# Performance work log

Hardware: AMD Instinct MI355X
Metric: run time of the kernel (lower is better)

Reference implementation:

```python
import jax, jax.numpy as jnp
import numpy as np

D_CONV = 4
DT_RANK = 64
D_STATE = 16

def silu(v):
    return v * jax.nn.sigmoid(v)

def setup_inputs() -> dict:
    key = jax.random.key(0)
    ks = jax.random.split(key, 10)
    B, L, d_model, d_inner = 2, 2048, 1024, 2048
    def nrm(k, shape, scale):
        return jax.random.normal(k, shape, dtype=jnp.float32) * scale
    A = jnp.tile(jnp.arange(1, D_STATE + 1, dtype=jnp.float32), (d_inner, 1))
    return {
        'x': nrm(ks[0], (B, L, d_model), 1.0),
        'W_in': nrm(ks[1], (d_model, 2 * d_inner), d_model ** -0.5),
        'conv_w': nrm(ks[2], (d_inner, D_CONV), D_CONV ** -0.5),
        'conv_b': nrm(ks[3], (d_inner,), 0.02),
        'W_x': nrm(ks[4], (d_inner, DT_RANK + 2 * D_STATE), d_inner ** -0.5),
        'W_dt': nrm(ks[5], (DT_RANK, d_inner), DT_RANK ** -0.5),
        'b_dt': nrm(ks[6], (d_inner,), 0.02),
        'A_log': jnp.log(A),
        'D': jnp.ones((d_inner,), dtype=jnp.float32),
        'W_out': nrm(ks[7], (d_inner, d_model), d_inner ** -0.5),
    }

def reference(x, W_in, conv_w, conv_b, W_x, W_dt, b_dt, A_log, D, W_out):
    B, L, _ = x.shape
    d_inner = W_dt.shape[1]
    # input projection and gate split
    xz = x @ W_in                                   # [B, L, 2*d_inner]
    xb, z = jnp.split(xz, 2, axis=-1)
    # causal depthwise conv1d (pad left d_conv-1, then first L outputs)
    xp = jnp.pad(xb, ((0, 0), (D_CONV - 1, 0), (0, 0)))
    xc = sum(xp[:, k:k + L, :] * conv_w[:, k] for k in range(D_CONV)) + conv_b
    xb = silu(xc)                                   # [B, L, d_inner]
    # data-dependent SSM parameters
    x_dbl = xb @ W_x                                # [B, L, dt_rank + 2*d_state]
    dt_low, Bm, Cm = jnp.split(x_dbl, [DT_RANK, DT_RANK + D_STATE], axis=-1)
    dt = jax.nn.softplus(dt_low @ W_dt + b_dt)      # [B, L, d_inner]
    A = -jnp.exp(A_log)                             # [d_inner, d_state]

    def step(h, inp):
        dt_t, B_t, C_t, x_t = inp                   # [B,d_inner],[B,n],[B,n],[B,d_inner]
        dA = jnp.exp(A * dt_t[..., None])           # [B, d_inner, d_state]
        h = h * dA + (x_t * dt_t)[..., None] * B_t[:, None, :]
        y = jnp.einsum('bdn,bn->bd', h, C_t)
        return h, y

    xs = (dt.swapaxes(0, 1), Bm.swapaxes(0, 1), Cm.swapaxes(0, 1), xb.swapaxes(0, 1))
    h0 = jnp.zeros((B, d_inner, D_STATE), dtype=x.dtype)
    _, ys = jax.lax.scan(step, h0, xs)              # ys: [L, B, d_inner]
    y = ys.swapaxes(0, 1) + xb * D
    out = y * silu(z)
    return out @ W_out
```

## Files before the change

kernel.cpp:

```cpp
#include <hip/hip_runtime.h>
#include <hip/hip_bf16.h>


#define BATCH   2
#define SEQLEN  2048
#define DMODEL  1024
#define DINNER  2048
#define DCONV   4
#define DTRANK  64
#define DSTATE  16
#define BL      (BATCH * SEQLEN)
#define NXZ     (2 * DINNER)
#define XDBL_N  (DTRANK + 2 * DSTATE)
#define LCH     32
#define NCHUNK  (SEQLEN / LCH)
#define KSPLIT  8
#define KC      (DINNER / KSPLIT)
#define ALDS    264
#define KS_OUT  4
#define KCO     (DINNER / KS_OUT)

typedef __bf16 bf16x8 __attribute__((ext_vector_type(8)));
typedef __bf16 bf16x4 __attribute__((ext_vector_type(4)));
typedef float  floatx4 __attribute__((ext_vector_type(4)));

__device__ __forceinline__ float silu_f(float v) {
    return v / (1.f + __expf(-v));
}

__device__ __forceinline__ float softplus_f(float v) {
    return (v > 20.f) ? v : __logf(1.f + __expf(v));
}

__device__ __forceinline__ float fast_exp2(float v) {
    return __builtin_amdgcn_exp2f(v);
}

__device__ __forceinline__ void gload_lds16(const __bf16* g, __bf16* l) {
    __builtin_amdgcn_global_load_lds(
        (const __attribute__((address_space(1))) void*)g,
        (__attribute__((address_space(3))) void*)l, 16, 0, 0);
}

#define VMW(n) asm volatile("s_waitcnt vmcnt(" #n ")" ::: "memory")
#define BARX() __builtin_amdgcn_s_barrier()

template <int BUF, int QA>
__device__ __forceinline__ void rdA(const char* rA, bf16x8 (&aF)[4][2]) {
#pragma unroll
    for (int j = 0; j < 4; ++j) {
        aF[j][0] = *(const bf16x8*)(rA + BUF * 65536 + ((QA * 4 + j) * 2 + 0) * 1024);
        aF[j][1] = *(const bf16x8*)(rA + BUF * 65536 + ((QA * 4 + j) * 2 + 1) * 1024);
    }
}

template <int BUF, int QB>
__device__ __forceinline__ void rdB(const char* rB, bf16x8 (&bF)[2][2]) {
#pragma unroll
    for (int f = 0; f < 2; ++f) {
        bF[f][0] = *(const bf16x8*)(rB + BUF * 65536 + QB * 8192 + f * 2048 + 0);
        bF[f][1] = *(const bf16x8*)(rB + BUF * 65536 + QB * 8192 + f * 2048 + 1024);
    }
}

template <int QA, int QB>
__device__ __forceinline__ void mf16(const bf16x8 (&aF)[4][2], const bf16x8 (&bF)[2][2],
                                     floatx4 (&acc)[8][4]) {
    __builtin_amdgcn_s_setprio(1);
#pragma unroll
    for (int ks = 0; ks < 2; ++ks)
#pragma unroll
        for (int j = 0; j < 4; ++j)
#pragma unroll
            for (int f = 0; f < 2; ++f)
                acc[QA * 4 + j][QB * 2 + f] = __builtin_amdgcn_mfma_f32_16x16x32_bf16(
                    aF[j][ks], bF[f][ks], acc[QA * 4 + j][QB * 2 + f], 0, 0, 0);
    __builtin_amdgcn_s_setprio(0);
}

template <int BUF, int QA>
__device__ __forceinline__ void stA2(const __bf16* gAs, char* sm, int lda, int w, int t) {
    gload_lds16(gAs + (size_t)(QA * 64) * lda + t * 64,
                (__bf16*)(sm + BUF * 65536 + QA * 8192 + w * 1024));
    gload_lds16(gAs + (size_t)(128 + QA * 64) * lda + t * 64,
                (__bf16*)(sm + BUF * 65536 + 16384 + QA * 8192 + w * 1024));
}

template <int BUF, int QB>
__device__ __forceinline__ void stB2(const __bf16* gBs, char* sm, int lda, int w, int t) {
    gload_lds16(gBs + (size_t)(QB * 32) * lda + t * 64,
                (__bf16*)(sm + BUF * 65536 + 32768 + QB * 8192 + w * 1024));
    gload_lds16(gBs + (size_t)(128 + QB * 32) * lda + t * 64,
                (__bf16*)(sm + BUF * 65536 + 32768 + 16384 + QB * 8192 + w * 1024));
}

template <int EPI>
__global__ __launch_bounds__(512, 2) void gemm_bt_256(
    const __bf16* __restrict__ A,
    const __bf16* __restrict__ BT,
    void* __restrict__ Cv,
    int M, int N, int K, int lda,
    const float* __restrict__ bias)
{
    __shared__ __align__(16) char smem[131072];

    const int tid  = threadIdx.x;
    const int w    = tid >> 6;
    const int lane = tid & 63;

    const int cpx = gridDim.x >> 3;
    const int swz = (blockIdx.x & 7) * cpx + (blockIdx.x >> 3);
    const int ntn = N >> 8;
    const int row0 = (swz / ntn) << 8;
    const int col0 = (swz % ntn) << 8;
    const int kbase = blockIdx.y * K;

    const int P     = tid;
    const int rr    = (P >> 2) & 15;
    const int qq    = (P & 3) ^ (2 * ((P >> 5) & 1));
    const int colE  = (((P >> 6) & 1) * 4 + qq) * 8;
    const int rgP   = P >> 7;
    const int rowAu = rgP * 16 + rr;
    const int rowBu = (rgP >> 1) * 64 + (rgP & 1) * 16 + rr;

    const __bf16* gAs = A  + (size_t)(row0 + rowAu) * lda + kbase + colE;
    const __bf16* gBs = BT + (size_t)(col0 + rowBu) * lda + kbase + colE;
    char* sm = smem;

    const int lsw = ((lane & 15) * 4 + ((lane >> 4) ^ (2 * ((lane >> 3) & 1)))) * 16;
    const char* rA = smem + (w >> 2) * 16384 + lsw;
    const char* rB = smem + 32768 + ((w & 3) >> 1) * 16384 + ((w & 3) & 1) * 4096 + lsw;

    floatx4 acc[8][4];
#pragma unroll
    for (int i = 0; i < 8; ++i)
#pragma unroll
        for (int j = 0; j < 4; ++j)
            acc[i][j] = (floatx4){0.f, 0.f, 0.f, 0.f};
    bf16x8 aF[4][2], bF[2][2];

    const int NT = K >> 6;
    const int NI = NT >> 1;

    stA2<0, 0>(gAs, sm, lda, w, 0);
    stB2<0, 0>(gBs, sm, lda, w, 0);
    stB2<0, 1>(gBs, sm, lda, w, 0);
    stA2<0, 1>(gAs, sm, lda, w, 0);
    stA2<1, 0>(gAs, sm, lda, w, 1);
    stB2<1, 1>(gBs, sm, lda, w, 1);
    VMW(6);
    BARX();

    for (int i = 0; i < NI - 1; ++i) {
        const int t1 = 2 * i + 1, t2 = 2 * i + 2, t3 = 2 * i + 3;
        rdA<0, 0>(rA, aF); rdB<0, 0>(rB, bF);
        stB2<1, 0>(gBs, sm, lda, w, t1);
        BARX(); mf16<0, 0>(aF, bF, acc); BARX();
        rdB<0, 1>(rB, bF);
        stA2<1, 1>(gAs, sm, lda, w, t1);
        BARX(); mf16<0, 1>(aF, bF, acc); VMW(8); BARX();
        rdA<0, 1>(rA, aF);
        stA2<0, 0>(gAs, sm, lda, w, t2);
        BARX(); mf16<1, 1>(aF, bF, acc); BARX();
        rdB<0, 0>(rB, bF);
        stB2<0, 1>(gBs, sm, lda, w, t2);
        BARX(); mf16<1, 0>(aF, bF, acc); VMW(6); BARX();
        rdA<1, 0>(rA, aF); rdB<1, 0>(rB, bF);
        stB2<0, 0>(gBs, sm, lda, w, t2);
        BARX(); mf16<0, 0>(aF, bF, acc); BARX();
        rdB<1, 1>(rB, bF);
        stA2<0, 1>(gAs, sm, lda, w, t2);
        BARX(); mf16<0, 1>(aF, bF, acc); VMW(8); BARX();
        rdA<1, 1>(rA, aF);
        stA2<1, 0>(gAs, sm, lda, w, t3);
        BARX(); mf16<1, 1>(aF, bF, acc); BARX();
        rdB<1, 0>(rB, bF);
        stB2<1, 1>(gBs, sm, lda, w, t3);
        BARX(); mf16<1, 0>(aF, bF, acc); VMW(6); BARX();
    }
    {
        const int t1 = NT - 1;
        rdA<0, 0>(rA, aF); rdB<0, 0>(rB, bF);
        stB2<1, 0>(gBs, sm, lda, w, t1);
        BARX(); mf16<0, 0>(aF, bF, acc); BARX();
        rdB<0, 1>(rB, bF);
        stA2<1, 1>(gAs, sm, lda, w, t1);
        BARX(); mf16<0, 1>(aF, bF, acc); VMW(8); BARX();
        rdA<0, 1>(rA, aF);
        BARX(); mf16<1, 1>(aF, bF, acc); BARX();
        rdB<0, 0>(rB, bF);
        BARX(); mf16<1, 0>(aF, bF, acc); VMW(2); BARX();
        rdA<1, 0>(rA, aF); rdB<1, 0>(rB, bF);
        BARX(); mf16<0, 0>(aF, bF, acc); BARX();
        rdB<1, 1>(rB, bF);
        BARX(); mf16<0, 1>(aF, bF, acc); VMW(0); BARX();
        rdA<1, 1>(rA, aF);
        BARX(); mf16<1, 1>(aF, bF, acc); BARX();
        rdB<1, 0>(rB, bF);
        BARX(); mf16<1, 0>(aF, bF, acc);
    }

    const int lrow = lane & 15, quad = lane >> 4;
    const int rbase = row0 + (w >> 2) * 128;
    const int cbase = col0 + (w & 3) * 64;
    const size_t cofs = (size_t)blockIdx.y * (size_t)M * (size_t)N;
#pragma unroll
    for (int fi = 0; fi < 8; ++fi) {
#pragma unroll
        for (int cf = 0; cf < 4; ++cf) {
            const int col = cbase + cf * 16 + lrow;
            const float bv = (EPI == 1 || EPI == 3) ? bias[col] : 0.f;
#pragma unroll
            for (int r = 0; r < 4; ++r) {
                const int row = rbase + fi * 16 + quad * 4 + r;
                float v = acc[fi][cf][r];
                if (EPI == 1 || EPI == 3) v = softplus_f(v + bv);
                if (EPI == 2 || EPI == 3)
                    ((__bf16*)Cv)[(size_t)row * N + col] = (__bf16)v;
                else
                    ((float*)Cv)[cofs + (size_t)row * N + col] = v;
            }
        }
    }
    (void)M;
}

__global__ __launch_bounds__(256) void out_reduce(
    const float* __restrict__ parts, float* __restrict__ out)
{
    const size_t i = ((size_t)blockIdx.x * 256 + threadIdx.x) * 4;
    floatx4 s = *(const floatx4*)(parts + i);
#pragma unroll
    for (int kz = 1; kz < KS_OUT; ++kz)
        s += *(const floatx4*)(parts + (size_t)kz * BL * DMODEL + i);
    *(floatx4*)(out + i) = s;
}

template <int EPI>
__global__ __launch_bounds__(256) void gemm_r64(
    const __bf16* __restrict__ A,
    const __bf16* __restrict__ BT,
    void* __restrict__ Cv,
    int M, int N, int K,
    const float* __restrict__ bias)
{
    __shared__ __bf16 Asm[64 * 32];
    __shared__ __bf16 Bsm[128 * 32];

    const int tid  = threadIdx.x;
    const int w    = tid >> 6;
    const int lane = tid & 63;
    const int lrow = lane & 15;
    const int quad = lane >> 4;
    const int row0 = blockIdx.y * 64;
    const int col0 = blockIdx.x * 128;
    const int wc   = w * 32;

    const int ldr = tid >> 2;
    const int ldk = (tid & 3) * 8;
    const __bf16* gA = A  + (size_t)(row0 + ldr) * K + ldk;
    const __bf16* gB = BT + (size_t)(col0 + ldr) * K + ldk;
    const size_t half = (size_t)64 * K;
    __bf16* lA0 = Asm + w * 512;
    __bf16* lB0 = Bsm + w * 512;
    __bf16* lB1 = Bsm + 2048 + w * 512;

    floatx4 acc[4][2];
#pragma unroll
    for (int i = 0; i < 4; ++i)
#pragma unroll
        for (int j = 0; j < 2; ++j)
            acc[i][j] = (floatx4){0.f, 0.f, 0.f, 0.f};

    for (int k0 = 0; k0 < K; k0 += 32) {
        gload_lds16(gA, lA0);
        gload_lds16(gB, lB0);
        gload_lds16(gB + half, lB1);
        gA += 32; gB += 32;
        __syncthreads();

        bf16x8 af[4], bf[2];
#pragma unroll
        for (int t = 0; t < 4; ++t)
            af[t] = *(const bf16x8*)(Asm + (t * 16 + lrow) * 32 + quad * 8);
#pragma unroll
        for (int u = 0; u < 2; ++u)
            bf[u] = *(const bf16x8*)(Bsm + (wc + u * 16 + lrow) * 32 + quad * 8);

#pragma unroll
        for (int ti = 0; ti < 4; ++ti)
#pragma unroll
            for (int tj = 0; tj < 2; ++tj)
                acc[ti][tj] = __builtin_amdgcn_mfma_f32_16x16x32_bf16(
                    af[ti], bf[tj], acc[ti][tj], 0, 0, 0);
        __syncthreads();
    }

#pragma unroll
    for (int ti = 0; ti < 4; ++ti) {
#pragma unroll
        for (int tj = 0; tj < 2; ++tj) {
            int col = col0 + wc + tj * 16 + lrow;
            float bv = (EPI == 1 || EPI == 3) ? bias[col] : 0.f;
#pragma unroll
            for (int r = 0; r < 4; ++r) {
                int row = row0 + ti * 16 + quad * 4 + r;
                float v = acc[ti][tj][r];
                if (EPI == 1 || EPI == 3) v = softplus_f(v + bv);
                if (EPI == 2 || EPI == 3)
                    ((__bf16*)Cv)[(size_t)row * N + col] = (__bf16)v;
                else
                    ((float*)Cv)[(size_t)row * N + col] = v;
            }
        }
    }
}

#define NB_CAST  ((BL * DMODEL / 4) / 256)
#define NB_WIN   ((NXZ / 32) * (DMODEL / 32))
#define NB_WOUT  ((DMODEL / 32) * (DINNER / 32))
#define NB_WDT   ((DINNER / 32) * (DTRANK / 32))
#define NB_CW    ((DCONV * DINNER) / 256)

__device__ __forceinline__ void transpose_tile(
    const float* __restrict__ src, __bf16* __restrict__ dst, int R, int Cc,
    int bx, int by, int tid, float* tile)
{
    int tx = tid & 31, ty = tid >> 5;
    int c0 = bx * 32, r0 = by * 32;
#pragma unroll
    for (int i = 0; i < 32; i += 8)
        tile[(ty + i) * 33 + tx] = src[(size_t)(r0 + ty + i) * Cc + c0 + tx];
    __syncthreads();
#pragma unroll
    for (int i = 0; i < 32; i += 8)
        dst[(size_t)(c0 + ty + i) * R + r0 + tx] = (__bf16)tile[tx * 33 + ty + i];
}

__global__ __launch_bounds__(256) void prep_kernel(
    const float* __restrict__ x,
    const float* __restrict__ W_in,
    const float* __restrict__ W_out,
    const float* __restrict__ W_dt,
    const float* __restrict__ conv_w,
    __bf16* __restrict__ xb16,
    __bf16* __restrict__ WiT16,
    __bf16* __restrict__ WoT16,
    __bf16* __restrict__ WdtT16,
    float* __restrict__ cwT)
{
    __shared__ float tile[32 * 33];
    const int tid = threadIdx.x;
    int bid = blockIdx.x;

    if (bid < NB_CAST) {
        long i = ((long)bid * 256 + tid) * 4;
        float4 v = *(const float4*)(x + i);
        bf16x4 o = {(__bf16)v.x, (__bf16)v.y, (__bf16)v.z, (__bf16)v.w};
        *(bf16x4*)(xb16 + i) = o;
        return;
    }
    bid -= NB_CAST;
    if (bid < NB_WIN) {
        transpose_tile(W_in, WiT16, DMODEL, NXZ,
                       bid % (NXZ / 32), bid / (NXZ / 32), tid, tile);
        return;
    }
    bid -= NB_WIN;
    if (bid < NB_WOUT) {
        transpose_tile(W_out, WoT16, DINNER, DMODEL,
                       bid % (DMODEL / 32), bid / (DMODEL / 32), tid, tile);
        return;
    }
    bid -= NB_WOUT;
    if (bid < NB_WDT) {
        transpose_tile(W_dt, WdtT16, DTRANK, DINNER,
                       bid % (DINNER / 32), bid / (DINNER / 32), tid, tile);
        return;
    }
    bid -= NB_WDT;
    {
        int i = bid * 256 + tid;
        int k = i / DINNER, d = i % DINNER;
        cwT[i] = conv_w[d * DCONV + k];
    }
}

__global__ __launch_bounds__(256) void xdbl_fused(
    const __bf16* __restrict__ xz16,
    const float* __restrict__ cwT,
    const float* __restrict__ cb,
    const float* __restrict__ W,
    __bf16* __restrict__ xc16,
    float* __restrict__ parts)
{
    __shared__ __bf16 Acv[64 * ALDS];
    __shared__ float Bs[16][97];

    const int tid  = threadIdx.x;
    const int row0 = blockIdx.x * 64;
    const int kz   = blockIdx.y;
    const int kbeg = kz * KC;

    {
        const int ct = (tid & 31) * 8;
        const int rt = (tid >> 5) * 8;
        const int d  = kbeg + ct;

        float wreg[DCONV][8];
#pragma unroll
        for (int k = 0; k < DCONV; ++k) {
            float4 a = *(const float4*)(cwT + k * DINNER + d);
            float4 b = *(const float4*)(cwT + k * DINNER + d + 4);
            wreg[k][0]=a.x; wreg[k][1]=a.y; wreg[k][2]=a.z; wreg[k][3]=a.w;
            wreg[k][4]=b.x; wreg[k][5]=b.y; wreg[k][6]=b.z; wreg[k][7]=b.w;
        }
        float bias8[8];
        {
            float4 a = *(const float4*)(cb + d);
            float4 b = *(const float4*)(cb + d + 4);
            bias8[0]=a.x; bias8[1]=a.y; bias8[2]=a.z; bias8[3]=a.w;
            bias8[4]=b.x; bias8[5]=b.y; bias8[6]=b.z; bias8[7]=b.w;
        }

        const bf16x8 zero = {};
        bf16x8 win[DCONV];
        const int tloc0 = (int)((row0 + rt) & (SEQLEN - 1));
#pragma unroll
        for (int j = 0; j < DCONV - 1; ++j)
            win[j] = (tloc0 - 3 + j >= 0)
                ? *(const bf16x8*)(xz16 + (size_t)(row0 + rt - 3 + j) * NXZ + d)
                : zero;

        for (int i = 0; i < 8; ++i) {
            size_t r = (size_t)row0 + rt + i;
            win[DCONV - 1] = *(const bf16x8*)(xz16 + r * NXZ + d);
            bf16x8 o;
#pragma unroll
            for (int j = 0; j < 8; ++j) {
                float acc = bias8[j];
#pragma unroll
                for (int k = 0; k < DCONV; ++k)
                    acc += (float)win[k][j] * wreg[k][j];
                o[j] = (__bf16)silu_f(acc);
            }
            *(bf16x8*)(Acv + (rt + i) * ALDS + ct) = o;
            *(bf16x8*)(xc16 + r * DINNER + d) = o;
#pragma unroll
            for (int k = 0; k < DCONV - 1; ++k)
                win[k] = win[k + 1];
        }
    }
    __syncthreads();

    const int tr = tid >> 4;
    const int tc = tid & 15;
    const int brow = tid >> 4;
    const int bcol = (tid & 15) * 6;

    float acc[4][6] = {};

    for (int k0 = 0; k0 < KC; k0 += 16) {
#pragma unroll
        for (int j = 0; j < 6; ++j)
            Bs[brow][bcol + j] = W[(size_t)(kbeg + k0 + brow) * XDBL_N + bcol + j];
        __syncthreads();

#pragma unroll
        for (int h = 0; h < 2; ++h) {
            float a8[4][8];
#pragma unroll
            for (int i = 0; i < 4; ++i) {
                bf16x8 av = *(const bf16x8*)(Acv + (tr * 4 + i) * ALDS + k0 + h * 8);
#pragma unroll
                for (int e = 0; e < 8; ++e) a8[i][e] = (float)av[e];
            }
#pragma unroll
            for (int kk = 0; kk < 8; ++kk) {
                float b6[6];
#pragma unroll
                for (int j = 0; j < 6; ++j) b6[j] = Bs[h * 8 + kk][tc * 6 + j];
#pragma unroll
                for (int i = 0; i < 4; ++i)
#pragma unroll
                    for (int j = 0; j < 6; ++j)
                        acc[i][j] += a8[i][kk] * b6[j];
            }
        }
        __syncthreads();
    }

    const long base = (long)kz * BL * XDBL_N;
#pragma unroll
    for (int i = 0; i < 4; ++i) {
        long off = base + (long)(row0 + tr * 4 + i) * XDBL_N + tc * 6;
#pragma unroll
        for (int j = 0; j < 6; ++j)
            parts[off + j] = acc[i][j];
    }
}

__global__ __launch_bounds__(256) void xdbl_reduce(
    const float* __restrict__ parts, float* __restrict__ xdbl,
    __bf16* __restrict__ dtlow16)
{
    long i = (long)blockIdx.x * 256 + threadIdx.x;
    float s = 0.f;
#pragma unroll
    for (int kz = 0; kz < KSPLIT; ++kz)
        s += parts[(long)kz * BL * XDBL_N + i];
    xdbl[i] = s;
    int col = (int)(i % XDBL_N);
    if (col < DTRANK) {
        long row = i / XDBL_N;
        dtlow16[row * DTRANK + col] = (__bf16)s;
    }
}

__global__ __launch_bounds__(256) void scan_pass1(
    const __bf16* __restrict__ dt16,
    const __bf16* __restrict__ xc16,
    const float* __restrict__ xdbl,
    const float* __restrict__ A_log,
    float* __restrict__ sums_h,
    float* __restrict__ sums_p)
{
    const int d  = blockIdx.x * 256 + threadIdx.x;
    const int bc = blockIdx.y;
    const int b  = bc / NCHUNK, c = bc % NCHUNK;
    const long r0 = (long)b * SEQLEN + (long)c * LCH;

    float Ad[DSTATE];
    {
        const float4* al = (const float4*)(A_log + d * DSTATE);
#pragma unroll
        for (int q = 0; q < 4; ++q) {
            float4 v = al[q];
            Ad[q * 4 + 0] = -__expf(v.x) * 1.44269504f;
            Ad[q * 4 + 1] = -__expf(v.y) * 1.44269504f;
            Ad[q * 4 + 2] = -__expf(v.z) * 1.44269504f;
            Ad[q * 4 + 3] = -__expf(v.w) * 1.44269504f;
        }
    }

    float h[DSTATE] = {};
    float Pp[DSTATE];
#pragma unroll
    for (int n = 0; n < DSTATE; ++n) Pp[n] = 1.f;

    for (int t = 0; t < LCH; ++t) {
        long r = r0 + t;
        float dtv = (float)dt16[r * DINNER + d];
        float xv  = (float)xc16[r * DINNER + d];
        float xdt = xv * dtv;
        const float4* bv = (const float4*)(xdbl + r * XDBL_N + DTRANK);
        float4 B0 = bv[0], B1 = bv[1], B2 = bv[2], B3 = bv[3];
        const float Bn[DSTATE] = {B0.x,B0.y,B0.z,B0.w, B1.x,B1.y,B1.z,B1.w,
                                  B2.x,B2.y,B2.z,B2.w, B3.x,B3.y,B3.z,B3.w};
#pragma unroll
        for (int n = 0; n < DSTATE; ++n) {
            float dA = fast_exp2(Ad[n] * dtv);
            h[n] = h[n] * dA + xdt * Bn[n];
            Pp[n] *= dA;
        }
    }

    const long rowbase = (long)bc * DSTATE;
#pragma unroll
    for (int n = 0; n < DSTATE; ++n) {
        sums_h[(rowbase + n) * DINNER + d] = h[n];
        sums_p[(rowbase + n) * DINNER + d] = Pp[n];
    }
}

__global__ __launch_bounds__(256) void scan_combine(
    float* __restrict__ sums_h, float* __restrict__ sums_p)
{
    int u = blockIdx.x * 256 + threadIdx.x;
    int d = u & (DINNER - 1);
    int n = (u >> 11) & (DSTATE - 1);
    int b = u >> 15;
    float hg = 0.f;
    for (int c = 0; c < NCHUNK; ++c) {
        long row = (long)(b * NCHUNK + c) * DSTATE + n;
        float p  = sums_p[row * DINNER + d];
        float hl = sums_h[row * DINNER + d];
        sums_p[row * DINNER + d] = hg;
        hg = p * hg + hl;
    }
}

__global__ __launch_bounds__(256) void scan_pass3(
    const __bf16* __restrict__ dt16,
    const __bf16* __restrict__ xc16,
    const float* __restrict__ xdbl,
    const float* __restrict__ A_log,
    const __bf16* __restrict__ xz16,
    const float* __restrict__ sums_p,
    const float* __restrict__ Dp,
    __bf16* __restrict__ gated)
{
    const int d  = blockIdx.x * 256 + threadIdx.x;
    const int bc = blockIdx.y;
    const int b  = bc / NCHUNK, c = bc % NCHUNK;
    const long r0 = (long)b * SEQLEN + (long)c * LCH;

    float Ad[DSTATE];
    {
        const float4* al = (const float4*)(A_log + d * DSTATE);
#pragma unroll
        for (int q = 0; q < 4; ++q) {
            float4 v = al[q];
            Ad[q * 4 + 0] = -__expf(v.x) * 1.44269504f;
            Ad[q * 4 + 1] = -__expf(v.y) * 1.44269504f;
            Ad[q * 4 + 2] = -__expf(v.z) * 1.44269504f;
            Ad[q * 4 + 3] = -__expf(v.w) * 1.44269504f;
        }
    }

    float h[DSTATE];
    const long rowbase = (long)bc * DSTATE;
#pragma unroll
    for (int n = 0; n < DSTATE; ++n)
        h[n] = sums_p[(rowbase + n) * DINNER + d];

    const float Dv = Dp[d];

    for (int t = 0; t < LCH; ++t) {
        long r = r0 + t;
        float dtv = (float)dt16[r * DINNER + d];
        float xv  = (float)xc16[r * DINNER + d];
        float xdt = xv * dtv;
        const float4* bv = (const float4*)(xdbl + r * XDBL_N + DTRANK);
        float4 B0 = bv[0], B1 = bv[1], B2 = bv[2], B3 = bv[3];
        float4 C0 = bv[4], C1 = bv[5], C2 = bv[6], C3 = bv[7];
        const float Bn[DSTATE] = {B0.x,B0.y,B0.z,B0.w, B1.x,B1.y,B1.z,B1.w,
                                  B2.x,B2.y,B2.z,B2.w, B3.x,B3.y,B3.z,B3.w};
        const float Cn[DSTATE] = {C0.x,C0.y,C0.z,C0.w, C1.x,C1.y,C1.z,C1.w,
                                  C2.x,C2.y,C2.z,C2.w, C3.x,C3.y,C3.z,C3.w};
        float y = 0.f;
#pragma unroll
        for (int n = 0; n < DSTATE; ++n) {
            float dA = fast_exp2(Ad[n] * dtv);
            h[n] = h[n] * dA + xdt * Bn[n];
            y += h[n] * Cn[n];
        }
        float z = (float)xz16[r * NXZ + DINNER + d];
        float yy = y + xv * Dv;
        gated[r * DINNER + d] = (__bf16)(yy * silu_f(z));
    }
}

extern "C" void kernel_launch(void* const* d_in, const int* in_sizes, int n_in,
                              void* d_out, int out_size, void* d_ws, size_t ws_size,
                              hipStream_t stream) {
    const float* x      = (const float*)d_in[0];
    const float* W_in   = (const float*)d_in[1];
    const float* conv_w = (const float*)d_in[2];
    const float* conv_b = (const float*)d_in[3];
    const float* W_x    = (const float*)d_in[4];
    const float* W_dt   = (const float*)d_in[5];
    const float* b_dt   = (const float*)d_in[6];
    const float* A_log  = (const float*)d_in[7];
    const float* Dp     = (const float*)d_in[8];
    const float* W_out  = (const float*)d_in[9];
    float* out = (float*)d_out;

    __bf16* xz16    = (__bf16*)d_ws;
    __bf16* xc16    = xz16 + (long)BL * NXZ;
    __bf16* dt16    = xc16 + (long)BL * DINNER;
    __bf16* gated16 = dt16 + (long)BL * DINNER;
    __bf16* WoT16   = gated16 + (long)BL * DINNER;
    __bf16* WdtT16  = WoT16 + (long)DINNER * DMODEL;
    __bf16* dtlow16 = WdtT16 + (long)DINNER * DTRANK;
    __bf16* xb16    = dtlow16 + (long)BL * DTRANK;
    __bf16* WiT16   = xb16 + (long)BL * DMODEL;
    float*  xdbl    = (float*)(WiT16 + (long)NXZ * DMODEL);
    float*  cwT     = xdbl + (long)BL * XDBL_N;
    float*  scratch = cwT + (long)DCONV * DINNER;
    float*  sums_h  = scratch;
    float*  sums_p  = scratch + (long)BATCH * NCHUNK * DSTATE * DINNER;
    float* outparts = (float*)d_ws;

    dim3 blk(256);

    prep_kernel<<<dim3(NB_CAST + NB_WIN + NB_WOUT + NB_WDT + NB_CW), blk, 0, stream>>>(
        x, W_in, W_out, W_dt, conv_w, xb16, WiT16, WoT16, WdtT16, cwT);

    gemm_bt_256<2><<<dim3((BL / 256) * (NXZ / 256)), dim3(512), 0, stream>>>(
        xb16, WiT16, xz16, BL, NXZ, DMODEL, DMODEL, nullptr);

    xdbl_fused<<<dim3(BL / 64, KSPLIT), blk, 0, stream>>>(
        xz16, cwT, conv_b, W_x, xc16, scratch);
    xdbl_reduce<<<dim3((BL * XDBL_N) / 256), blk, 0, stream>>>(scratch, xdbl, dtlow16);

    gemm_r64<3><<<dim3(DINNER / 128, BL / 64), blk, 0, stream>>>(
        dtlow16, WdtT16, dt16, BL, DINNER, DTRANK, b_dt);

    {
        dim3 grid1(DINNER / 256, BATCH * NCHUNK);
        scan_pass1<<<grid1, blk, 0, stream>>>(dt16, xc16, xdbl, A_log, sums_h, sums_p);
        scan_combine<<<dim3((BATCH * DSTATE * DINNER) / 256), blk, 0, stream>>>(
            sums_h, sums_p);
        scan_pass3<<<grid1, blk, 0, stream>>>(dt16, xc16, xdbl, A_log, xz16,
                                              sums_p, Dp, gated16);
    }
    gemm_bt_256<0><<<dim3((BL / 256) * (DMODEL / 256), KS_OUT), dim3(512), 0, stream>>>(
        gated16, WoT16, outparts, BL, DMODEL, KCO, DINNER, nullptr);
    out_reduce<<<dim3((BL * DMODEL) / 1024), blk, 0, stream>>>(outparts, out);

    (void)in_sizes; (void)n_in; (void)out_size; (void)ws_size;
}
```

Baseline: 291.8 us.

## Split conv from x_dbl projection and run projection on bf16 MFMA

The fused conv+projection kernel, which computed the x_dbl projection with scalar fp32 FMAs from shared memory, is split into two kernels. The first does the depthwise conv+SiLU and transposes W_x to bf16. The second is a split-K MFMA bf16 GEMM that reads xc16 back from global memory, with N padded to 128 and a vectorized reduce. This is meant to replace slow SIMT FMA work with matrix cores, at the cost of an extra launch, a reread of the conv output, and W_x rounded to bf16. The transposed W_x reuses the xb16 buffer, and the padded rows read leftover data whose outputs are dropped.

```diff
diff --git a/kernel.cpp b/kernel.cpp
--- a/kernel.cpp
+++ b/kernel.cpp
@@ -16,9 +16,11 @@
 #define NCHUNK  (SEQLEN / LCH)
 #define KSPLIT  8
 #define KC      (DINNER / KSPLIT)
-#define ALDS    264
 #define KS_OUT  4
 #define KCO     (DINNER / KS_OUT)
+#define KS_XD   8
+#define KCX     (DINNER / KS_XD)
+#define XDP     128
 
 typedef __bf16 bf16x8 __attribute__((ext_vector_type(8)));
 typedef __bf16 bf16x4 __attribute__((ext_vector_type(4)));
@@ -316,6 +318,97 @@
     }
 }
 
+__global__ __launch_bounds__(256) void xdbl_gemm(
+    const __bf16* __restrict__ A,
+    const __bf16* __restrict__ BT,
+    float* __restrict__ parts)
+{
+    __shared__ __bf16 Asm[64 * 32];
+    __shared__ __bf16 Bsm[128 * 32];
+
+    const int tid  = threadIdx.x;
+    const int w    = tid >> 6;
+    const int lane = tid & 63;
+    const int lrow = lane & 15;
+    const int quad = lane >> 4;
+    const int row0 = blockIdx.x * 64;
+    const int kbeg = blockIdx.y * KCX;
+    const int wc   = w * 32;
+
+    const int ldr = tid >> 2;
+    const int ldk = (tid & 3) * 8;
+    const __bf16* gA = A  + (size_t)(row0 + ldr) * DINNER + kbeg + ldk;
+    const __bf16* gB = BT + (size_t)ldr * DINNER + kbeg + ldk;
+    const size_t half = (size_t)64 * DINNER;
+    __bf16* lA0 = Asm + w * 512;
+    __bf16* lB0 = Bsm + w * 512;
+    __bf16* lB1 = Bsm + 2048 + w * 512;
+
+    floatx4 acc[4][2];
+#pragma unroll
+    for (int i = 0; i < 4; ++i)
+#pragma unroll
+        for (int j = 0; j < 2; ++j)
+            acc[i][j] = (floatx4){0.f, 0.f, 0.f, 0.f};
+
+    for (int k0 = 0; k0 < KCX; k0 += 32) {
+        gload_lds16(gA, lA0);
+        gload_lds16(gB, lB0);
+        gload_lds16(gB + half, lB1);
+        gA += 32; gB += 32;
+        __syncthreads();
+
+        bf16x8 af[4], bf[2];
+#pragma unroll
+        for (int t = 0; t < 4; ++t)
+            af[t] = *(const bf16x8*)(Asm + (t * 16 + lrow) * 32 + quad * 8);
+#pragma unroll
+        for (int u = 0; u < 2; ++u)
+            bf[u] = *(const bf16x8*)(Bsm + (wc + u * 16 + lrow) * 32 + quad * 8);
+
+#pragma unroll
+        for (int ti = 0; ti < 4; ++ti)
+#pragma unroll
+            for (int tj = 0; tj < 2; ++tj)
+                acc[ti][tj] = __builtin_amdgcn_mfma_f32_16x16x32_bf16(
+                    af[ti], bf[tj], acc[ti][tj], 0, 0, 0);
+        __syncthreads();
+    }
+
+    const size_t base = (size_t)blockIdx.y * BL * XDP;
+#pragma unroll
+    for (int ti = 0; ti < 4; ++ti) {
+#pragma unroll
+        for (int tj = 0; tj < 2; ++tj) {
+            int col = wc + tj * 16 + lrow;
+#pragma unroll
+            for (int r = 0; r < 4; ++r) {
+                int row = row0 + ti * 16 + quad * 4 + r;
+                parts[base + (size_t)row * XDP + col] = acc[ti][tj][r];
+            }
+        }
+    }
+}
+
+__global__ __launch_bounds__(256) void xdbl_reduce2(
+    const float* __restrict__ parts, float* __restrict__ xdbl,
+    __bf16* __restrict__ dtlow16)
+{
+    const int i4  = blockIdx.x * 256 + threadIdx.x;
+    const int row = i4 / 24;
+    const int c4  = i4 - row * 24;
+    const float* p = parts + (size_t)row * XDP + c4 * 4;
+    floatx4 s = *(const floatx4*)p;
+#pragma unroll
+    for (int kz = 1; kz < KS_XD; ++kz)
+        s += *(const floatx4*)(p + (size_t)kz * BL * XDP);
+    *(floatx4*)(xdbl + (size_t)row * XDBL_N + c4 * 4) = s;
+    if (c4 < 16) {
+        bf16x4 o = {(__bf16)s.x, (__bf16)s.y, (__bf16)s.z, (__bf16)s.w};
+        *(bf16x4*)(dtlow16 + (size_t)row * DTRANK + c4 * 4) = o;
+    }
+}
+
 #define NB_CAST  ((BL * DMODEL / 4) / 256)
 #define NB_WIN   ((NXZ / 32) * (DMODEL / 32))
 #define NB_WOUT  ((DMODEL / 32) * (DINNER / 32))
@@ -386,134 +479,75 @@
     }
 }
 
-__global__ __launch_bounds__(256) void xdbl_fused(
+#define NB_CONV  ((BL / 64) * KSPLIT)
+#define NB_WXT   ((DINNER / 32) * (XDBL_N / 32))
+
+__global__ __launch_bounds__(256) void conv_prep(
     const __bf16* __restrict__ xz16,
     const float* __restrict__ cwT,
     const float* __restrict__ cb,
-    const float* __restrict__ W,
+    const float* __restrict__ W_x,
     __bf16* __restrict__ xc16,
-    float* __restrict__ parts)
-{
-    __shared__ __bf16 Acv[64 * ALDS];
-    __shared__ float Bs[16][97];
-
-    const int tid  = threadIdx.x;
-    const int row0 = blockIdx.x * 64;
-    const int kz   = blockIdx.y;
-    const int kbeg = kz * KC;
-
+    __bf16* __restrict__ WxT16)
+{
+    __shared__ float tile[32 * 33];
+    const int tid = threadIdx.x;
+    const int bid = blockIdx.x;
+
+    if (bid >= NB_CONV) {
+        const int b2 = bid - NB_CONV;
+        transpose_tile(W_x, WxT16, DINNER, XDBL_N,
+                       b2 % (XDBL_N / 32), b2 / (XDBL_N / 32), tid, tile);
+        return;
+    }
+
+    const int row0 = (bid >> 3) * 64;
+    const int kbeg = (bid & 7) * KC;
+    const int ct = (tid & 31) * 8;
+    const int rt = (tid >> 5) * 8;
+    const int d  = kbeg + ct;
+
+    float wreg[DCONV][8];
+#pragma unroll
+    for (int k = 0; k < DCONV; ++k) {
+        float4 a = *(const float4*)(cwT + k * DINNER + d);
+        float4 b = *(const float4*)(cwT + k * DINNER + d + 4);
+        wreg[k][0]=a.x; wreg[k][1]=a.y; wreg[k][2]=a.z; wreg[k][3]=a.w;
+        wreg[k][4]=b.x; wreg[k][5]=b.y; wreg[k][6]=b.z; wreg[k][7]=b.w;
+    }
+    float bias8[8];
     {
-        const int ct = (tid & 31) * 8;
-        const int rt = (tid >> 5) * 8;
-        const int d  = kbeg + ct;
-
-        float wreg[DCONV][8];
-#pragma unroll
-        for (int k = 0; k < DCONV; ++k) {
-            float4 a = *(const float4*)(cwT + k * DINNER + d);
-            float4 b = *(const float4*)(cwT + k * DINNER + d + 4);
-            wreg[k][0]=a.x; wreg[k][1]=a.y; wreg[k][2]=a.z; wreg[k][3]=a.w;
-            wreg[k][4]=b.x; wreg[k][5]=b.y; wreg[k][6]=b.z; wreg[k][7]=b.w;
+        float4 a = *(const float4*)(cb + d);
+        float4 b = *(const float4*)(cb + d + 4);
+        bias8[0]=a.x; bias8[1]=a.y; bias8[2]=a.z; bias8[3]=a.w;
+        bias8[4]=b.x; bias8[5]=b.y; bias8[6]=b.z; bias8[7]=b.w;
+    }
+
+    const bf16x8 zero = {};
+    bf16x8 win[DCONV];
+    const int tloc0 = (int)((row0 + rt) & (SEQLEN - 1));
+#pragma unroll
+    for (int j = 0; j < DCONV - 1; ++j)
+        win[j] = (tloc0 - 3 + j >= 0)
+            ? *(const bf16x8*)(xz16 + (size_t)(row0 + rt - 3 + j) * NXZ + d)
+            : zero;
+
+    for (int i = 0; i < 8; ++i) {
+        size_t r = (size_t)row0 + rt + i;
+        win[DCONV - 1] = *(const bf16x8*)(xz16 + r * NXZ + d);
+        bf16x8 o;
+#pragma unroll
+        for (int j = 0; j < 8; ++j) {
+            float acc = bias8[j];
+#pragma unroll
+            for (int k = 0; k < DCONV; ++k)
+                acc += (float)win[k][j] * wreg[k][j];
+            o[j] = (__bf16)silu_f(acc);
         }
-        float bias8[8];
-        {
-            float4 a = *(const float4*)(cb + d);
-            float4 b = *(const float4*)(cb + d + 4);
-            bias8[0]=a.x; bias8[1]=a.y; bias8[2]=a.z; bias8[3]=a.w;
-            bias8[4]=b.x; bias8[5]=b.y; bias8[6]=b.z; bias8[7]=b.w;
-        }
-
-        const bf16x8 zero = {};
-        bf16x8 win[DCONV];
-        const int tloc0 = (int)((row0 + rt) & (SEQLEN - 1));
-#pragma unroll
-        for (int j = 0; j < DCONV - 1; ++j)
-            win[j] = (tloc0 - 3 + j >= 0)
-                ? *(const bf16x8*)(xz16 + (size_t)(row0 + rt - 3 + j) * NXZ + d)
-                : zero;
-
-        for (int i = 0; i < 8; ++i) {
-            size_t r = (size_t)row0 + rt + i;
-            win[DCONV - 1] = *(const bf16x8*)(xz16 + r * NXZ + d);
-            bf16x8 o;
-#pragma unroll
-            for (int j = 0; j < 8; ++j) {
-                float acc = bias8[j];
-#pragma unroll
-                for (int k = 0; k < DCONV; ++k)
-                    acc += (float)win[k][j] * wreg[k][j];
-                o[j] = (__bf16)silu_f(acc);
-            }
-            *(bf16x8*)(Acv + (rt + i) * ALDS + ct) = o;
-            *(bf16x8*)(xc16 + r * DINNER + d) = o;
-#pragma unroll
-            for (int k = 0; k < DCONV - 1; ++k)
-                win[k] = win[k + 1];
-        }
-    }
-    __syncthreads();
-
-    const int tr = tid >> 4;
-    const int tc = tid & 15;
-    const int brow = tid >> 4;
-    const int bcol = (tid & 15) * 6;
-
-    float acc[4][6] = {};
-
-    for (int k0 = 0; k0 < KC; k0 += 16) {
-#pragma unroll
-        for (int j = 0; j < 6; ++j)
-            Bs[brow][bcol + j] = W[(size_t)(kbeg + k0 + brow) * XDBL_N + bcol + j];
-        __syncthreads();
-
-#pragma unroll
-        for (int h = 0; h < 2; ++h) {
-            float a8[4][8];
-#pragma unroll
-            for (int i = 0; i < 4; ++i) {
-                bf16x8 av = *(const bf16x8*)(Acv + (tr * 4 + i) * ALDS + k0 + h * 8);
-#pragma unroll
-                for (int e = 0; e < 8; ++e) a8[i][e] = (float)av[e];
-            }
-#pragma unroll
-            for (int kk = 0; kk < 8; ++kk) {
-                float b6[6];
-#pragma unroll
-                for (int j = 0; j < 6; ++j) b6[j] = Bs[h * 8 + kk][tc * 6 + j];
-#pragma unroll
-                for (int i = 0; i < 4; ++i)
-#pragma unroll
-                    for (int j = 0; j < 6; ++j)
-                        acc[i][j] += a8[i][kk] * b6[j];
-            }
-        }
-        __syncthreads();
-    }
-
-    const long base = (long)kz * BL * XDBL_N;
-#pragma unroll
-    for (int i = 0; i < 4; ++i) {
-        long off = base + (long)(row0 + tr * 4 + i) * XDBL_N + tc * 6;
-#pragma unroll
-        for (int j = 0; j < 6; ++j)
-            parts[off + j] = acc[i][j];
-    }
-}
-
-__global__ __launch_bounds__(256) void xdbl_reduce(
-    const float* __restrict__ parts, float* __restrict__ xdbl,
-    __bf16* __restrict__ dtlow16)
-{
-    long i = (long)blockIdx.x * 256 + threadIdx.x;
-    float s = 0.f;
-#pragma unroll
-    for (int kz = 0; kz < KSPLIT; ++kz)
-        s += parts[(long)kz * BL * XDBL_N + i];
-    xdbl[i] = s;
-    int col = (int)(i % XDBL_N);
-    if (col < DTRANK) {
-        long row = i / XDBL_N;
-        dtlow16[row * DTRANK + col] = (__bf16)s;
+        *(bf16x8*)(xc16 + r * DINNER + d) = o;
+#pragma unroll
+        for (int k = 0; k < DCONV - 1; ++k)
+            win[k] = win[k + 1];
     }
 }
 
@@ -680,6 +714,7 @@
     float*  scratch = cwT + (long)DCONV * DINNER;
     float*  sums_h  = scratch;
     float*  sums_p  = scratch + (long)BATCH * NCHUNK * DSTATE * DINNER;
+    __bf16* WxT16 = xb16;
     float* outparts = (float*)d_ws;
 
     dim3 blk(256);
@@ -690,9 +725,11 @@
     gemm_bt_256<2><<<dim3((BL / 256) * (NXZ / 256)), dim3(512), 0, stream>>>(
         xb16, WiT16, xz16, BL, NXZ, DMODEL, DMODEL, nullptr);
 
-    xdbl_fused<<<dim3(BL / 64, KSPLIT), blk, 0, stream>>>(
-        xz16, cwT, conv_b, W_x, xc16, scratch);
-    xdbl_reduce<<<dim3((BL * XDBL_N) / 256), blk, 0, stream>>>(scratch, xdbl, dtlow16);
+    conv_prep<<<dim3(NB_CONV + NB_WXT), blk, 0, stream>>>(
+        xz16, cwT, conv_b, W_x, xc16, WxT16);
+
+    xdbl_gemm<<<dim3(BL / 64, KS_XD), blk, 0, stream>>>(xc16, WxT16, scratch);
+    xdbl_reduce2<<<dim3((BL * 24) / 256), blk, 0, stream>>>(scratch, xdbl, dtlow16);
 
     gemm_r64<3><<<dim3(DINNER / 128, BL / 64), blk, 0, stream>>>(
         dtlow16, WdtT16, dt16, BL, DINNER, DTRANK, b_dt);
```

New measurement: 278.7 us. 4.5% less time.
